# Kernel optimization log

Measured on AMD Instinct MI355X. Metric: run time of the kernel, lower is better.

The kernel has to match this reference:

```python
import jax, jax.numpy as jnp
import numpy as np

D_MODEL = 768
N_HEADS = 12
HEAD_DIM = D_MODEL // N_HEADS
FFN_DIM = 3072
MAX_WAVELENGTH = 10000.0
ROPE_PERCENT = 0.5
NORM_EPS = 1e-5


def setup_inputs() -> dict:
    key = jax.random.key(0)
    ks = jax.random.split(key, 12)
    B, C, S = 2, 16, 128
    init = lambda k, shape: (jax.random.normal(k, shape, dtype=jnp.float32) * 0.02)
    return {
        "hidden_state": jax.random.normal(ks[0], (B, C, S, D_MODEL), dtype=jnp.float32),
        "wq": init(ks[1], (D_MODEL, D_MODEL)), "bq": jnp.zeros((D_MODEL,), jnp.float32),
        "wk": init(ks[2], (D_MODEL, D_MODEL)), "bk": jnp.zeros((D_MODEL,), jnp.float32),
        "wv": init(ks[3], (D_MODEL, D_MODEL)), "bv": jnp.zeros((D_MODEL,), jnp.float32),
        "wo": init(ks[4], (D_MODEL, D_MODEL)), "bo": jnp.zeros((D_MODEL,), jnp.float32),
        "attn_biases": init(ks[5], (N_HEADS, 2)),
        "ln1_g": jnp.ones((D_MODEL,), jnp.float32), "ln1_b": jnp.zeros((D_MODEL,), jnp.float32),
        "ln3_g": jnp.ones((D_MODEL,), jnp.float32), "ln3_b": jnp.zeros((D_MODEL,), jnp.float32),
        "w1": init(ks[6], (D_MODEL, FFN_DIM)), "b1": jnp.zeros((FFN_DIM,), jnp.float32),
        "w2": init(ks[7], (FFN_DIM, D_MODEL)), "b2": jnp.zeros((D_MODEL,), jnp.float32),
    }


def _layernorm(x, g, b):
    mu = jnp.mean(x, axis=-1, keepdims=True)
    var = jnp.mean(jnp.square(x - mu), axis=-1, keepdims=True)
    return (x - mu) * jax.lax.rsqrt(var + NORM_EPS) * g + b


def _apply_p_rope(x, positions):
    # x: [B, H, T, head_dim]; p-RoPE: only rope_percent of frequency bands rotate.
    half = HEAD_DIM // 2
    rope_angles = int(ROPE_PERCENT * HEAD_DIM) // 2  # 16
    fraction = 2.0 * jnp.arange(rope_angles, dtype=jnp.float32) / HEAD_DIM
    timescale = jnp.concatenate([
        MAX_WAVELENGTH ** fraction,
        jnp.full((half - rope_angles,), jnp.inf, dtype=jnp.float32),
    ])  # [half]
    angles = positions[:, None].astype(jnp.float32) / timescale[None, :]  # [T, half]
    sin = jnp.sin(angles)[None, None]  # [1,1,T,half]
    cos = jnp.cos(angles)[None, None]
    x1, x2 = jnp.split(x, 2, axis=-1)
    return jnp.concatenate([x1 * cos - x2 * sin, x2 * cos + x1 * sin], axis=-1)


def _forward(hidden_state, wq, bq, wk, bk, wv, bv, wo, bo, attn_biases,
             ln1_g, ln1_b, ln3_g, ln3_b, w1, b1, w2, b2):
    B, C, S, D = hidden_state.shape
    T = C * S
    flat = hidden_state.reshape(B, T, D)

    # --- attention sublayer (pre-norm) ---
    ni = _layernorm(flat, ln1_g, ln1_b)
    scaling = HEAD_DIM ** -0.5
    q = (ni @ wq + bq) * scaling
    k = ni @ wk + bk
    v = ni @ wv + bv
    to_heads = lambda t: t.reshape(B, T, N_HEADS, HEAD_DIM).transpose(0, 2, 1, 3)
    q, k, v = to_heads(q), to_heads(k), to_heads(v)  # [B,H,T,hd]

    positions = jnp.arange(T)
    k = _apply_p_rope(k, positions)
    q = _apply_p_rope(q, positions)

    scores = jnp.einsum("bhtd,bhsd->bhts", q, k)  # [B,H,T,T]
    variate_ids = positions // S
    same = (variate_ids[:, None] == variate_ids[None, :]).astype(scores.dtype)  # [T,T]
    variate_bias = (same[None, :, :] * attn_biases[:, 0][:, None, None]
                    + (1.0 - same[None, :, :]) * attn_biases[:, 1][:, None, None])  # [H,T,T]
    scores = scores + variate_bias[None]
    probs = jax.nn.softmax(scores, axis=-1)
    attn = jnp.einsum("bhts,bhsd->bhtd", probs, v)
    attn = attn.transpose(0, 2, 1, 3).reshape(B, T, D)
    attn = attn @ wo + bo

    flat = flat + attn  # residual (pre-norm -> no post-norm here)

    # --- feed-forward sublayer (pre-norm) ---
    ff_in = _layernorm(flat, ln3_g, ln3_b)
    ff = jax.nn.gelu(ff_in @ w1 + b1, approximate=False) @ w2 + b2
    flat = flat + ff

    return flat.reshape(B, C, S, D)


def reference(hidden_state, wq, bq, wk, bk, wv, bv, wo, bo, attn_biases,
              ln1_g, ln1_b, ln3_g, ln3_b, w1, b1, w2, b2):
    return _forward(hidden_state, wq, bq, wk, bk, wv, bv, wo, bo, attn_biases,
                    ln1_g, ln1_b, ln3_g, ln3_b, w1, b1, w2, b2)
```

## Files before the change

kernel.cpp:

```cpp
#include <hip/hip_runtime.h>
#include <cmath>


typedef __bf16 bf16_t;
typedef bf16_t bf16x8 __attribute__((ext_vector_type(8)));
typedef float floatx4 __attribute__((ext_vector_type(4)));

#define MFMA(a, b, c) __builtin_amdgcn_mfma_f32_16x16x32_bf16((a), (b), (c), 0, 0, 0)
#define LOG2E 1.44269504088896340736f

__device__ __forceinline__ bf16_t f2bf(float f) { return (bf16_t)f; }

__device__ __forceinline__ void g2l16(const void* g, void* l) {
  __builtin_amdgcn_global_load_lds(
      (const __attribute__((address_space(1))) unsigned int*)g,
      (__attribute__((address_space(3))) unsigned int*)l, 16, 0, 0);
}

__device__ __forceinline__ void lds_fence() {
  asm volatile("s_waitcnt lgkmcnt(0)" ::: "memory");
}

struct PrepP {
  const float *wq, *wk, *wv, *wo, *w1, *w2;
  bf16_t *wqkvT, *woT, *w1T, *w2T;
  const float *hs, *g1, *be1;
  bf16_t* ni;
};

__global__ __launch_bounds__(256) void k_prep(PrepP p) {
  __shared__ float shm[32 * 33];
  const int bid = blockIdx.x;
  if (bid < 6912) {
    const float* in;
    bf16_t* out;
    int R, C, tx, ty;
    if (bid < 2304) {
      int m = bid / 576, lo = bid % 576;
      in = (m == 0) ? p.wq : (m == 1) ? p.wk : (m == 2) ? p.wv : p.wo;
      out = (m < 3) ? p.wqkvT + (size_t)m * 768 * 768 : p.woT;
      R = 768; C = 768; tx = lo % 24; ty = lo / 24;
    } else if (bid < 4608) {
      int lo = bid - 2304;
      in = p.w1; out = p.w1T; R = 768; C = 3072; tx = lo % 96; ty = lo / 96;
    } else {
      int lo = bid - 4608;
      in = p.w2; out = p.w2T; R = 3072; C = 768; tx = lo % 24; ty = lo / 24;
    }
    const int c0 = tx * 32, r0 = ty * 32;
    const int lx = threadIdx.x & 31, ly = threadIdx.x >> 5;
#pragma unroll
    for (int p4 = 0; p4 < 4; p4++) {
      int r = ly + p4 * 8;
      shm[r * 33 + lx] = in[(size_t)(r0 + r) * C + c0 + lx];
    }
    __syncthreads();
#pragma unroll
    for (int p4 = 0; p4 < 4; p4++) {
      int r = ly + p4 * 8;
      out[(size_t)(c0 + r) * R + r0 + lx] = f2bf(shm[lx * 33 + r]);
    }
  } else {
    const int row = bid - 6912;
    const float* xr = p.hs + (size_t)row * 768;
    const int t = threadIdx.x;
    float v0 = xr[t], v1 = xr[t + 256], v2 = xr[t + 512];
    float s = v0 + v1 + v2;
    float s2 = v0 * v0 + v1 * v1 + v2 * v2;
#pragma unroll
    for (int off = 32; off; off >>= 1) {
      s += __shfl_xor(s, off);
      s2 += __shfl_xor(s2, off);
    }
    const int w = t >> 6;
    if ((t & 63) == 0) { shm[w] = s; shm[4 + w] = s2; }
    __syncthreads();
    s = shm[0] + shm[1] + shm[2] + shm[3];
    s2 = shm[4] + shm[5] + shm[6] + shm[7];
    const float mu = s * (1.0f / 768.0f);
    const float var = s2 * (1.0f / 768.0f) - mu * mu;
    const float rstd = rsqrtf(var + 1e-5f);
    bf16_t* orow = p.ni + (size_t)row * 768;
    orow[t]       = f2bf((v0 - mu) * rstd * p.g1[t]       + p.be1[t]);
    orow[t + 256] = f2bf((v1 - mu) * rstd * p.g1[t + 256] + p.be1[t + 256]);
    orow[t + 512] = f2bf((v2 - mu) * rstd * p.g1[t + 512] + p.be1[t + 512]);
  }
}

__global__ __launch_bounds__(256) void k_layernorm(
    const float* __restrict__ x, const float* __restrict__ g,
    const float* __restrict__ b, bf16_t* __restrict__ out) {
  const int row = blockIdx.x;
  const float* xr = x + (size_t)row * 768;
  const int t = threadIdx.x;
  float v0 = xr[t], v1 = xr[t + 256], v2 = xr[t + 512];
  float s = v0 + v1 + v2;
  float s2 = v0 * v0 + v1 * v1 + v2 * v2;
#pragma unroll
  for (int off = 32; off; off >>= 1) {
    s += __shfl_xor(s, off);
    s2 += __shfl_xor(s2, off);
  }
  __shared__ float ra[4], rb[4];
  const int w = t >> 6;
  if ((t & 63) == 0) { ra[w] = s; rb[w] = s2; }
  __syncthreads();
  s = ra[0] + ra[1] + ra[2] + ra[3];
  s2 = rb[0] + rb[1] + rb[2] + rb[3];
  const float mu = s * (1.0f / 768.0f);
  const float var = s2 * (1.0f / 768.0f) - mu * mu;
  const float rstd = rsqrtf(var + 1e-5f);
  bf16_t* orow = out + (size_t)row * 768;
  orow[t]       = f2bf((v0 - mu) * rstd * g[t]       + b[t]);
  orow[t + 256] = f2bf((v1 - mu) * rstd * g[t + 256] + b[t + 256]);
  orow[t + 512] = f2bf((v2 - mu) * rstd * g[t + 512] + b[t + 512]);
}

struct GemmP {
  const bf16_t* A;
  const bf16_t* Bt;
  int M, N, K, mode;
  const float* bias0;
  const float* bias1;
  const float* bias2;
  float* outF;
  bf16_t* outB0;
  bf16_t* outB1;
  bf16_t* outB2;
};

__global__ __launch_bounds__(256, 3) void k_gemm(GemmP p) {
  __shared__ bf16_t lds[18432];
  const int tid = threadIdx.x;
  const int lane = tid & 63, wave = tid >> 6;
  const int quad = lane >> 4, l15 = lane & 15;
  const int wm = (wave >> 1) * 64, wn = (wave & 1) * 64;
  const int m0 = blockIdx.y * 128, n0 = blockIdx.x * 128;

  const char* gA[4];
  const char* gB[4];
#pragma unroll
  for (int pp = 0; pp < 4; pp++) {
    int slot = wave * 256 + pp * 64 + lane;
    int r = slot >> 3;
    int c8 = ((slot & 7) ^ (r & 7)) << 3;
    gA[pp] = (const char*)(p.A + (size_t)(m0 + r) * p.K + c8);
    gB[pp] = (const char*)(p.Bt + (size_t)(n0 + r) * p.K + c8);
  }

  int offA[4], offB[4];
#pragma unroll
  for (int i = 0; i < 4; i++) {
    int ra = wm + i * 16 + l15;
    offA[i] = ra * 64 + ((quad * 8) ^ ((ra & 7) << 3));
    int rb = wn + i * 16 + l15;
    offB[i] = rb * 64 + ((quad * 8) ^ ((rb & 7) << 3));
  }

  const floatx4 z4 = {0.f, 0.f, 0.f, 0.f};
  floatx4 acc[4][4];
#pragma unroll
  for (int i = 0; i < 4; i++)
#pragma unroll
    for (int j = 0; j < 4; j++) acc[i][j] = z4;

  const int KT = p.K >> 6;
  bf16_t* Ad = lds + wave * 2048;
  bf16_t* Bd = lds + 8192 + wave * 2048;

  for (int kt = 0; kt < KT; kt++) {
    const size_t kb = (size_t)kt * 128;
#pragma unroll
    for (int pp = 0; pp < 4; pp++) {
      g2l16(gA[pp] + kb, Ad + pp * 512);
      g2l16(gB[pp] + kb, Bd + pp * 512);
    }
    __syncthreads();
#pragma unroll
    for (int ks = 0; ks < 2; ks++) {
      bf16x8 af[4], bfr[4];
#pragma unroll
      for (int i = 0; i < 4; i++) {
        af[i] = *(const bf16x8*)(lds + (offA[i] ^ (ks * 32)));
        bfr[i] = *(const bf16x8*)(lds + 8192 + (offB[i] ^ (ks * 32)));
      }
#pragma unroll
      for (int i = 0; i < 4; i++)
#pragma unroll
        for (int j = 0; j < 4; j++) acc[i][j] = MFMA(af[i], bfr[j], acc[i][j]);
    }
    __syncthreads();
  }

  char* scr = (char*)lds + wave * 9216;

  if (p.mode == 0) {
    const int gnw = n0 + wn;
    const int region = gnw / 768;
    const int rem = gnw - region * 768;
    const int h = rem >> 6;
    const int b = (m0 + wm) >> 11;
    const int t0 = (m0 + wm) & 2047;
    const float* bias = (region == 0) ? p.bias0 : (region == 1 ? p.bias1 : p.bias2);
    float bb[4];
#pragma unroll
    for (int j = 0; j < 4; j++) bb[j] = bias[h * 64 + j * 16 + l15];
    bf16_t* sb = (bf16_t*)scr;
    if (region < 2) {
      const float scale = (region == 0) ? 0.125f * LOG2E : 1.0f;
      const float inv_ts = exp2f(-(float)l15 * (13.287712379549449f / 32.0f));
#pragma unroll
      for (int i = 0; i < 4; i++) {
#pragma unroll
        for (int reg = 0; reg < 4; reg++) {
          int tl = i * 16 + quad * 4 + reg;
          float sn, cs;
          __sincosf((float)(t0 + tl) * inv_ts, &sn, &cs);
          float v0 = (acc[i][0][reg] + bb[0]) * scale;
          float v1 = (acc[i][1][reg] + bb[1]) * scale;
          float v2 = (acc[i][2][reg] + bb[2]) * scale;
          float v3 = (acc[i][3][reg] + bb[3]) * scale;
          sb[tl * 72 + l15]      = f2bf(v0 * cs - v2 * sn);
          sb[tl * 72 + 16 + l15] = f2bf(v1);
          sb[tl * 72 + 32 + l15] = f2bf(v2 * cs + v0 * sn);
          sb[tl * 72 + 48 + l15] = f2bf(v3);
        }
      }
      __syncthreads();
      bf16_t* outp = (region == 0) ? p.outB0 : p.outB1;
      bf16_t* ob = outp + (((size_t)(b * 12 + h) * 2048 + t0) << 6);
#pragma unroll
      for (int pp = 0; pp < 8; pp++) {
        int row = pp * 8 + (lane >> 3), ch = (lane & 7) << 3;
        *(bf16x8*)(ob + row * 64 + ch) = *(const bf16x8*)&sb[row * 72 + ch];
      }
    } else {
#pragma unroll
      for (int i = 0; i < 4; i++)
#pragma unroll
        for (int j = 0; j < 4; j++)
#pragma unroll
          for (int reg = 0; reg < 4; reg++)
            sb[(j * 16 + l15) * 72 + i * 16 + quad * 4 + reg] =
                f2bf(acc[i][j][reg] + bb[j]);
      __syncthreads();
      bf16_t* ob = p.outB2 + (((size_t)(b * 12 + h)) << 17) + t0;
#pragma unroll
      for (int pp = 0; pp < 8; pp++) {
        int d = pp * 8 + (lane >> 3), ch = (lane & 7) << 3;
        *(bf16x8*)(ob + (size_t)d * 2048 + ch) = *(const bf16x8*)&sb[d * 72 + ch];
      }
    }
  } else {
    bf16_t* sb = (bf16_t*)scr;
    float bb[4];
#pragma unroll
    for (int j = 0; j < 4; j++) bb[j] = p.bias0[n0 + wn + j * 16 + l15];
#pragma unroll
    for (int i = 0; i < 4; i++)
#pragma unroll
      for (int j = 0; j < 4; j++)
#pragma unroll
        for (int reg = 0; reg < 4; reg++) {
          int tl = i * 16 + quad * 4 + reg;
          float x = acc[i][j][reg] + bb[j];
          float gv = 0.5f * x * (1.0f + erff(x * 0.70710678118654752f));
          sb[tl * 72 + j * 16 + l15] = f2bf(gv);
        }
    __syncthreads();
#pragma unroll
    for (int pp = 0; pp < 8; pp++) {
      int row = pp * 8 + (lane >> 3), ch = (lane & 7) << 3;
      *(bf16x8*)(p.outB0 + (size_t)(m0 + wm + row) * p.N + n0 + wn + ch) =
          *(const bf16x8*)&sb[row * 72 + ch];
    }
  }
}

__global__ __launch_bounds__(256, 4) void k_gemm64(
    const bf16_t* __restrict__ A, const bf16_t* __restrict__ Bt, int N, int K,
    const float* __restrict__ bias, const float* __restrict__ resid,
    float* __restrict__ outF) {
  __shared__ bf16_t lds[16384];
  const int tid = threadIdx.x;
  const int lane = tid & 63, wave = tid >> 6;
  const int quad = lane >> 4, l15 = lane & 15;
  const int wm = (wave >> 1) * 32, wn = (wave & 1) * 32;
  const int m0 = blockIdx.y * 64, n0 = blockIdx.x * 64;

  const char* gA[4];
  const char* gB[4];
#pragma unroll
  for (int pp = 0; pp < 4; pp++) {
    int slot = wave * 256 + pp * 64 + lane;
    int r = slot >> 4;
    int c = ((slot & 15) ^ (r & 7)) << 3;
    gA[pp] = (const char*)(A + (size_t)(m0 + r) * K + c);
    gB[pp] = (const char*)(Bt + (size_t)(n0 + r) * K + c);
  }

  const floatx4 z4 = {0.f, 0.f, 0.f, 0.f};
  floatx4 acc[2][2];
#pragma unroll
  for (int i = 0; i < 2; i++)
#pragma unroll
    for (int j = 0; j < 2; j++) acc[i][j] = z4;

  const int KT = K >> 7;
  bf16_t* Ad = lds + wave * 2048;
  bf16_t* Bd = lds + 8192 + wave * 2048;

  for (int kt = 0; kt < KT; kt++) {
    const size_t kb = (size_t)kt * 256;
#pragma unroll
    for (int pp = 0; pp < 4; pp++) {
      g2l16(gA[pp] + kb, Ad + pp * 512);
      g2l16(gB[pp] + kb, Bd + pp * 512);
    }
    __syncthreads();
#pragma unroll
    for (int ks = 0; ks < 4; ks++) {
      bf16x8 af[2], bfr[2];
#pragma unroll
      for (int i = 0; i < 2; i++) {
        int ra = wm + i * 16 + l15;
        af[i] = *(const bf16x8*)(lds + ra * 128 +
                                 (((ks * 4 + quad) ^ (ra & 7)) << 3));
        int rb = wn + i * 16 + l15;
        bfr[i] = *(const bf16x8*)(lds + 8192 + rb * 128 +
                                  (((ks * 4 + quad) ^ (rb & 7)) << 3));
      }
#pragma unroll
      for (int i = 0; i < 2; i++)
#pragma unroll
        for (int j = 0; j < 2; j++) acc[i][j] = MFMA(af[i], bfr[j], acc[i][j]);
    }
    __syncthreads();
  }

  float* s4 = (float*)lds + wave * 1024;
#pragma unroll
  for (int i = 0; i < 2; i++)
#pragma unroll
    for (int j = 0; j < 2; j++)
#pragma unroll
      for (int reg = 0; reg < 4; reg++)
        s4[(i * 16 + quad * 4 + reg) * 32 + j * 16 + l15] = acc[i][j][reg];
  __syncthreads();
#pragma unroll
  for (int pp = 0; pp < 4; pp++) {
    int row = pp * 8 + (lane >> 3);
    int c4 = (lane & 7) * 4;
    floatx4 v = *(const floatx4*)&s4[row * 32 + c4];
    size_t goff = (size_t)(m0 + wm + row) * N + n0 + wn + c4;
    floatx4 rv = *(const floatx4*)(resid + goff);
    floatx4 bv = *(const floatx4*)(bias + n0 + wn + c4);
    *(floatx4*)(outF + goff) = v + rv + bv;
  }
}

__global__ __launch_bounds__(256, 3) void k_flash(
    const bf16_t* __restrict__ qh, const bf16_t* __restrict__ kh,
    const bf16_t* __restrict__ vt, const float* __restrict__ ab,
    bf16_t* __restrict__ attnA) {
  __shared__ bf16_t sm[20480];
  bf16_t* lK = sm;
  bf16_t* lV = sm + 8192;
  bf16_t* lP = sm + 16384;

  const int tid = threadIdx.x, lane = tid & 63, wave = tid >> 6;
  const int quad = lane >> 4, l15 = lane & 15;
  const int qtile = blockIdx.x, bh = blockIdx.y;
  const int h = bh % 12, bq = bh / 12;
  const int qr0 = qtile * 64 + wave * 16;

  const bf16_t* Qb = qh + (size_t)bh * 2048 * 64;
  const bf16_t* Kb = kh + (size_t)bh * 2048 * 64;
  const bf16_t* Vb = vt + (size_t)bh * 64 * 2048;

  const char* gK[2];
  const char* gV[2];
#pragma unroll
  for (int pp = 0; pp < 2; pp++) {
    int slot = wave * 128 + pp * 64 + lane;
    int r = slot >> 3;
    int c8 = ((slot & 7) ^ (r & 7)) << 3;
    gK[pp] = (const char*)(Kb + r * 64 + c8);
    gV[pp] = (const char*)(Vb + (size_t)r * 2048 + c8);
  }

  bf16x8 qf[2];
#pragma unroll
  for (int ks = 0; ks < 2; ks++)
    qf[ks] = *(const bf16x8*)(Qb + (size_t)(qr0 + l15) * 64 + ks * 32 + quad * 8);

  int offK[4];
#pragma unroll
  for (int t4 = 0; t4 < 4; t4++) {
    int sr = t4 * 16 + l15;
    offK[t4] = sr * 64 + ((quad * 8) ^ ((sr & 7) << 3));
  }
  const int offP = l15 * 64 + ((quad * 8) ^ ((l15 & 7) << 3));

  const floatx4 z4 = {0.f, 0.f, 0.f, 0.f};
  float l_all[4] = {0.f, 0.f, 0.f, 0.f};
  floatx4 oacc[4];
#pragma unroll
  for (int dt = 0; dt < 4; dt++) oacc[dt] = z4;

  const float bc_same = ab[h * 2] * LOG2E;
  const float bc_diff = ab[h * 2 + 1] * LOG2E;
  const int myv = qtile >> 1;

  {
    bf16_t* K0 = lK + wave * 1024;
    bf16_t* V0 = lV + wave * 1024;
#pragma unroll
    for (int pp = 0; pp < 2; pp++) {
      g2l16(gK[pp], K0 + pp * 512);
      g2l16(gV[pp], V0 + pp * 512);
    }
  }
  __syncthreads();

  for (int kv = 0; kv < 32; kv++) {
    const int cur = kv & 1;
    if (kv + 1 < 32) {
      bf16_t* K1 = lK + (cur ^ 1) * 4096 + wave * 1024;
      bf16_t* V1 = lV + (cur ^ 1) * 4096 + wave * 1024;
      const size_t kb = (size_t)(kv + 1) * 8192, vb = (size_t)(kv + 1) * 128;
#pragma unroll
      for (int pp = 0; pp < 2; pp++) {
        g2l16(gK[pp] + kb, K1 + pp * 512);
        g2l16(gV[pp] + vb, V1 + pp * 512);
      }
    }
    const bf16_t* K0 = lK + cur * 4096;
    const bf16_t* V0 = lV + cur * 4096;

    floatx4 sacc[4] = {z4, z4, z4, z4};
#pragma unroll
    for (int ks = 0; ks < 2; ks++)
#pragma unroll
      for (int ct = 0; ct < 4; ct++)
        sacc[ct] = MFMA(qf[ks], *(const bf16x8*)(K0 + (offK[ct] ^ (ks * 32))),
                        sacc[ct]);

    const float bc = ((kv >> 1) == myv) ? bc_same : bc_diff;
#pragma unroll
    for (int ct = 0; ct < 4; ct++)
#pragma unroll
      for (int reg = 0; reg < 4; reg++) {
        float pv = exp2f(sacc[ct][reg] + bc);
        sacc[ct][reg] = pv;
        l_all[reg] += pv;
      }

    bf16_t* myP = lP + wave * 1024;
#pragma unroll
    for (int ct = 0; ct < 4; ct++)
#pragma unroll
      for (int reg = 0; reg < 4; reg++) {
        int r = quad * 4 + reg, s = ct * 16 + l15;
        myP[r * 64 + (((s >> 3) ^ (r & 7)) << 3) + (s & 7)] =
            f2bf(sacc[ct][reg]);
      }
    lds_fence();

#pragma unroll
    for (int ks = 0; ks < 2; ks++) {
      bf16x8 pf = *(const bf16x8*)(myP + (offP ^ (ks * 32)));
#pragma unroll
      for (int dt = 0; dt < 4; dt++)
        oacc[dt] = MFMA(pf, *(const bf16x8*)(V0 + (offK[dt] ^ (ks * 32))),
                        oacc[dt]);
    }
    __syncthreads();
  }

  float inv_l[4];
#pragma unroll
  for (int reg = 0; reg < 4; reg++) {
    float la = l_all[reg];
    la += __shfl_xor(la, 1); la += __shfl_xor(la, 2);
    la += __shfl_xor(la, 4); la += __shfl_xor(la, 8);
    inv_l[reg] = 1.0f / la;
  }

  bf16_t* myP = lP + wave * 1024;
#pragma unroll
  for (int dt = 0; dt < 4; dt++)
#pragma unroll
    for (int reg = 0; reg < 4; reg++)
      myP[(quad * 4 + reg) * 64 + dt * 16 + l15] =
          f2bf(oacc[dt][reg] * inv_l[reg]);
  __syncthreads();
#pragma unroll
  for (int pp = 0; pp < 2; pp++) {
    int row = pp * 8 + (lane >> 3), ch = (lane & 7) << 3;
    *(bf16x8*)(attnA + ((size_t)(bq * 2048 + qr0 + row)) * 768 + h * 64 + ch) =
        *(const bf16x8*)&myP[row * 64 + ch];
  }
}

extern "C" void kernel_launch(void* const* d_in, const int* in_sizes, int n_in,
                              void* d_out, int out_size, void* d_ws,
                              size_t ws_size, hipStream_t stream) {
  const float* hs  = (const float*)d_in[0];
  const float* wq  = (const float*)d_in[1];
  const float* bq  = (const float*)d_in[2];
  const float* wk  = (const float*)d_in[3];
  const float* bk  = (const float*)d_in[4];
  const float* wv  = (const float*)d_in[5];
  const float* bv  = (const float*)d_in[6];
  const float* wo  = (const float*)d_in[7];
  const float* bo  = (const float*)d_in[8];
  const float* ab  = (const float*)d_in[9];
  const float* g1  = (const float*)d_in[10];
  const float* be1 = (const float*)d_in[11];
  const float* g3  = (const float*)d_in[12];
  const float* be3 = (const float*)d_in[13];
  const float* w1  = (const float*)d_in[14];
  const float* b1  = (const float*)d_in[15];
  const float* w2  = (const float*)d_in[16];
  const float* b2  = (const float*)d_in[17];

  char* ws = (char*)d_ws;
  size_t off = 0;
  auto alloc = [&](size_t bytes) -> void* {
    void* p = ws + off;
    off += (bytes + 255) & ~(size_t)255;
    return p;
  };
  bf16_t* wqkvT = (bf16_t*)alloc((size_t)2304 * 768 * 2);
  bf16_t* woT   = (bf16_t*)alloc((size_t)768 * 768 * 2);
  bf16_t* w1T   = (bf16_t*)alloc((size_t)3072 * 768 * 2);
  bf16_t* w2T   = (bf16_t*)alloc((size_t)768 * 3072 * 2);
  bf16_t* ni    = (bf16_t*)alloc((size_t)4096 * 768 * 2);
  bf16_t* qhB   = (bf16_t*)alloc((size_t)24 * 2048 * 64 * 2);
  bf16_t* khB   = (bf16_t*)alloc((size_t)24 * 2048 * 64 * 2);
  bf16_t* vtB   = (bf16_t*)alloc((size_t)24 * 64 * 2048 * 2);
  bf16_t* attnA = (bf16_t*)alloc((size_t)4096 * 768 * 2);
  float*  resid1 = (float*)alloc((size_t)4096 * 768 * 4);
  bf16_t* ffn1o = qhB;

  PrepP pp = {wq, wk, wv, wo, w1, w2, wqkvT, woT, w1T, w2T, hs, g1, be1, ni};
  k_prep<<<11008, 256, 0, stream>>>(pp);

  GemmP gqkv = {ni, wqkvT, 4096, 2304, 768, 0,
                bq, bk, bv, nullptr, qhB, khB, vtB};
  k_gemm<<<dim3(18, 32), 256, 0, stream>>>(gqkv);

  k_flash<<<dim3(32, 24), 256, 0, stream>>>(qhB, khB, vtB, ab, attnA);

  k_gemm64<<<dim3(12, 64), 256, 0, stream>>>(attnA, woT, 768, 768, bo, hs,
                                             resid1);

  k_layernorm<<<4096, 256, 0, stream>>>(resid1, g3, be3, ni);

  GemmP gf1 = {ni, w1T, 4096, 3072, 768, 2,
               b1, nullptr, nullptr, nullptr, ffn1o, nullptr, nullptr};
  k_gemm<<<dim3(24, 32), 256, 0, stream>>>(gf1);

  k_gemm64<<<dim3(12, 64), 256, 0, stream>>>(ffn1o, w2T, 768, 3072, b2,
                                             resid1, (float*)d_out);
}
```

Baseline: 290.8 us.

## Rewrite flash attention with 32x32 MFMA, two-wave blocks, transposed S

The flash kernel now uses 32x32x16 bf16 MFMA instructions with 128-thread blocks, where each wave owns 32 query rows. Scores are computed transposed (K as the A operand), so each lane holds one query column and the row-sum reduction shrinks to a single shuffle. The K/V double buffering is removed in favour of a single buffer with a barrier per tile, and P is packed and stored as bf16x4. Fewer, larger MFMAs and a smaller LDS footprint are traded against losing the overlap of global loads with compute.

```diff
diff --git a/kernel.cpp b/kernel.cpp
--- a/kernel.cpp
+++ b/kernel.cpp
@@ -3,10 +3,13 @@
 
 
 typedef __bf16 bf16_t;
+typedef bf16_t bf16x4 __attribute__((ext_vector_type(4)));
 typedef bf16_t bf16x8 __attribute__((ext_vector_type(8)));
 typedef float floatx4 __attribute__((ext_vector_type(4)));
+typedef float floatx16 __attribute__((ext_vector_type(16)));
 
 #define MFMA(a, b, c) __builtin_amdgcn_mfma_f32_16x16x32_bf16((a), (b), (c), 0, 0, 0)
+#define MFMA32(a, b, c) __builtin_amdgcn_mfma_f32_32x32x16_bf16((a), (b), (c), 0, 0, 0)
 #define LOG2E 1.44269504088896340736f
 
 __device__ __forceinline__ bf16_t f2bf(float f) { return (bf16_t)f; }
@@ -359,147 +362,119 @@
   }
 }
 
-__global__ __launch_bounds__(256, 3) void k_flash(
+__global__ __launch_bounds__(128, 2) void k_flash(
     const bf16_t* __restrict__ qh, const bf16_t* __restrict__ kh,
     const bf16_t* __restrict__ vt, const float* __restrict__ ab,
     bf16_t* __restrict__ attnA) {
-  __shared__ bf16_t sm[20480];
+  __shared__ bf16_t sm[12288];
   bf16_t* lK = sm;
-  bf16_t* lV = sm + 8192;
-  bf16_t* lP = sm + 16384;
+  bf16_t* lV = sm + 4096;
+  bf16_t* lP = sm + 8192;
 
   const int tid = threadIdx.x, lane = tid & 63, wave = tid >> 6;
-  const int quad = lane >> 4, l15 = lane & 15;
+  const int l31 = lane & 31, lh = lane >> 5;
+  const int sw = l31 & 7;
   const int qtile = blockIdx.x, bh = blockIdx.y;
   const int h = bh % 12, bq = bh / 12;
-  const int qr0 = qtile * 64 + wave * 16;
+  const int qw = qtile * 64 + wave * 32;
 
   const bf16_t* Qb = qh + (size_t)bh * 2048 * 64;
   const bf16_t* Kb = kh + (size_t)bh * 2048 * 64;
   const bf16_t* Vb = vt + (size_t)bh * 64 * 2048;
 
-  const char* gK[2];
-  const char* gV[2];
-#pragma unroll
-  for (int pp = 0; pp < 2; pp++) {
-    int slot = wave * 128 + pp * 64 + lane;
+  const char* gK[4];
+  const char* gV[4];
+#pragma unroll
+  for (int pp = 0; pp < 4; pp++) {
+    int slot = pp * 128 + tid;
     int r = slot >> 3;
     int c8 = ((slot & 7) ^ (r & 7)) << 3;
     gK[pp] = (const char*)(Kb + r * 64 + c8);
     gV[pp] = (const char*)(Vb + (size_t)r * 2048 + c8);
   }
 
-  bf16x8 qf[2];
-#pragma unroll
-  for (int ks = 0; ks < 2; ks++)
-    qf[ks] = *(const bf16x8*)(Qb + (size_t)(qr0 + l15) * 64 + ks * 32 + quad * 8);
-
-  int offK[4];
-#pragma unroll
-  for (int t4 = 0; t4 < 4; t4++) {
-    int sr = t4 * 16 + l15;
-    offK[t4] = sr * 64 + ((quad * 8) ^ ((sr & 7) << 3));
-  }
-  const int offP = l15 * 64 + ((quad * 8) ^ ((l15 & 7) << 3));
-
-  const floatx4 z4 = {0.f, 0.f, 0.f, 0.f};
-  float l_all[4] = {0.f, 0.f, 0.f, 0.f};
-  floatx4 oacc[4];
-#pragma unroll
-  for (int dt = 0; dt < 4; dt++) oacc[dt] = z4;
+  bf16x8 qf[4];
+#pragma unroll
+  for (int ks = 0; ks < 4; ks++)
+    qf[ks] = *(const bf16x8*)(Qb + (size_t)(qw + l31) * 64 + ks * 16 + lh * 8);
+
+  const floatx16 z16 = {0.f, 0.f, 0.f, 0.f, 0.f, 0.f, 0.f, 0.f,
+                        0.f, 0.f, 0.f, 0.f, 0.f, 0.f, 0.f, 0.f};
+  floatx16 oacc0 = z16, oacc1 = z16;
+  float l_part = 0.f;
 
   const float bc_same = ab[h * 2] * LOG2E;
   const float bc_diff = ab[h * 2 + 1] * LOG2E;
   const int myv = qtile >> 1;
 
-  {
-    bf16_t* K0 = lK + wave * 1024;
-    bf16_t* V0 = lV + wave * 1024;
-#pragma unroll
-    for (int pp = 0; pp < 2; pp++) {
-      g2l16(gK[pp], K0 + pp * 512);
-      g2l16(gV[pp], V0 + pp * 512);
-    }
-  }
-  __syncthreads();
+  bf16_t* myP = lP + wave * 2048;
 
   for (int kv = 0; kv < 32; kv++) {
-    const int cur = kv & 1;
-    if (kv + 1 < 32) {
-      bf16_t* K1 = lK + (cur ^ 1) * 4096 + wave * 1024;
-      bf16_t* V1 = lV + (cur ^ 1) * 4096 + wave * 1024;
-      const size_t kb = (size_t)(kv + 1) * 8192, vb = (size_t)(kv + 1) * 128;
-#pragma unroll
-      for (int pp = 0; pp < 2; pp++) {
-        g2l16(gK[pp] + kb, K1 + pp * 512);
-        g2l16(gV[pp] + vb, V1 + pp * 512);
+    const size_t kb = (size_t)kv * 8192, vb = (size_t)kv * 128;
+#pragma unroll
+    for (int pp = 0; pp < 4; pp++) {
+      g2l16(gK[pp] + kb, lK + pp * 1024 + wave * 512);
+      g2l16(gV[pp] + vb, lV + pp * 1024 + wave * 512);
+    }
+    __syncthreads();
+
+    floatx16 sacc0 = z16, sacc1 = z16;
+#pragma unroll
+    for (int ks = 0; ks < 4; ks++) {
+      const int ch = ((2 * ks + lh) ^ sw) << 3;
+      sacc0 = MFMA32(*(const bf16x8*)(lK + l31 * 64 + ch), qf[ks], sacc0);
+      sacc1 = MFMA32(*(const bf16x8*)(lK + (32 + l31) * 64 + ch), qf[ks], sacc1);
+    }
+
+    const float bc = ((kv >> 1) == myv) ? bc_same : bc_diff;
+#pragma unroll
+    for (int st = 0; st < 2; st++) {
+      const floatx16& sv = st ? sacc1 : sacc0;
+#pragma unroll
+      for (int g = 0; g < 4; g++) {
+        bf16x4 pk;
+#pragma unroll
+        for (int r = 0; r < 4; r++) {
+          float pv = exp2f(sv[g * 4 + r] + bc);
+          l_part += pv;
+          pk[r] = f2bf(pv);
+        }
+        *(bf16x4*)(myP + l31 * 64 + (((st * 4 + g) ^ sw) << 3) + 4 * lh) = pk;
       }
     }
-    const bf16_t* K0 = lK + cur * 4096;
-    const bf16_t* V0 = lV + cur * 4096;
-
-    floatx4 sacc[4] = {z4, z4, z4, z4};
-#pragma unroll
-    for (int ks = 0; ks < 2; ks++)
-#pragma unroll
-      for (int ct = 0; ct < 4; ct++)
-        sacc[ct] = MFMA(qf[ks], *(const bf16x8*)(K0 + (offK[ct] ^ (ks * 32))),
-                        sacc[ct]);
-
-    const float bc = ((kv >> 1) == myv) ? bc_same : bc_diff;
-#pragma unroll
-    for (int ct = 0; ct < 4; ct++)
-#pragma unroll
-      for (int reg = 0; reg < 4; reg++) {
-        float pv = exp2f(sacc[ct][reg] + bc);
-        sacc[ct][reg] = pv;
-        l_all[reg] += pv;
-      }
-
-    bf16_t* myP = lP + wave * 1024;
-#pragma unroll
-    for (int ct = 0; ct < 4; ct++)
-#pragma unroll
-      for (int reg = 0; reg < 4; reg++) {
-        int r = quad * 4 + reg, s = ct * 16 + l15;
-        myP[r * 64 + (((s >> 3) ^ (r & 7)) << 3) + (s & 7)] =
-            f2bf(sacc[ct][reg]);
-      }
     lds_fence();
 
 #pragma unroll
-    for (int ks = 0; ks < 2; ks++) {
-      bf16x8 pf = *(const bf16x8*)(myP + (offP ^ (ks * 32)));
-#pragma unroll
-      for (int dt = 0; dt < 4; dt++)
-        oacc[dt] = MFMA(pf, *(const bf16x8*)(V0 + (offK[dt] ^ (ks * 32))),
-                        oacc[dt]);
-    }
-    __syncthreads();
-  }
-
-  float inv_l[4];
-#pragma unroll
-  for (int reg = 0; reg < 4; reg++) {
-    float la = l_all[reg];
-    la += __shfl_xor(la, 1); la += __shfl_xor(la, 2);
-    la += __shfl_xor(la, 4); la += __shfl_xor(la, 8);
-    inv_l[reg] = 1.0f / la;
-  }
-
-  bf16_t* myP = lP + wave * 1024;
-#pragma unroll
-  for (int dt = 0; dt < 4; dt++)
-#pragma unroll
-    for (int reg = 0; reg < 4; reg++)
-      myP[(quad * 4 + reg) * 64 + dt * 16 + l15] =
-          f2bf(oacc[dt][reg] * inv_l[reg]);
-  __syncthreads();
-#pragma unroll
-  for (int pp = 0; pp < 2; pp++) {
-    int row = pp * 8 + (lane >> 3), ch = (lane & 7) << 3;
-    *(bf16x8*)(attnA + ((size_t)(bq * 2048 + qr0 + row)) * 768 + h * 64 + ch) =
-        *(const bf16x8*)&myP[row * 64 + ch];
+    for (int ks = 0; ks < 4; ks++) {
+      const int ch = ((2 * ks + lh) ^ sw) << 3;
+      const bf16x8 pf = *(const bf16x8*)(myP + l31 * 64 + ch);
+      oacc0 = MFMA32(*(const bf16x8*)(lV + l31 * 64 + ch), pf, oacc0);
+      oacc1 = MFMA32(*(const bf16x8*)(lV + (32 + l31) * 64 + ch), pf, oacc1);
+    }
+    __syncthreads();
+  }
+
+  const float l_tot = l_part + __shfl_xor(l_part, 32);
+  const float inv = 1.0f / l_tot;
+
+  lds_fence();
+#pragma unroll
+  for (int dt = 0; dt < 2; dt++) {
+    const floatx16& ov = dt ? oacc1 : oacc0;
+#pragma unroll
+    for (int g = 0; g < 4; g++) {
+      bf16x4 pk;
+#pragma unroll
+      for (int r = 0; r < 4; r++) pk[r] = f2bf(ov[g * 4 + r] * inv);
+      *(bf16x4*)(myP + l31 * 64 + (((dt * 4 + g) ^ sw) << 3) + 4 * lh) = pk;
+    }
+  }
+  lds_fence();
+#pragma unroll
+  for (int ps = 0; ps < 4; ps++) {
+    int rr = ps * 8 + (lane >> 3), c = lane & 7;
+    bf16x8 v = *(const bf16x8*)(myP + rr * 64 + (((c ^ (rr & 7)) << 3)));
+    *(bf16x8*)(attnA + ((size_t)(bq * 2048 + qw + rr)) * 768 + h * 64 + c * 8) = v;
   }
 }
 
@@ -551,7 +526,7 @@
                 bq, bk, bv, nullptr, qhB, khB, vtB};
   k_gemm<<<dim3(18, 32), 256, 0, stream>>>(gqkv);
 
-  k_flash<<<dim3(32, 24), 256, 0, stream>>>(qhB, khB, vtB, ab, attnA);
+  k_flash<<<dim3(32, 24), 128, 0, stream>>>(qhB, khB, vtB, ab, attnA);
 
   k_gemm64<<<dim3(12, 64), 256, 0, stream>>>(attnA, woT, 768, 768, bo, hs,
                                              resid1);
```

Result: slower. 302.9 us (+4.2%).

## Split-K the FFN down-projection with atomic accumulation and remap block order

Applied to the files above, without the earlier changes.

Replaces the 64x64-tile down-projection GEMM (K=3072) with a 128x128-tile split-K kernel that divides K into four chunks and accumulates partial results into the output with float atomics. The first chunk also adds bias and residual, and the output is zeroed by a memset. Separately, block indices in the GEMM kernels are remapped column-major so consecutive blocks share B tiles, aiming for better L2 reuse. The split-K path adds atomic traffic, an extra memset, and a single-buffered K loop with no load/compute overlap.

```diff
diff --git a/kernel.cpp b/kernel.cpp
--- a/kernel.cpp
+++ b/kernel.cpp
@@ -135,7 +135,9 @@
   const int lane = tid & 63, wave = tid >> 6;
   const int quad = lane >> 4, l15 = lane & 15;
   const int wm = (wave >> 1) * 64, wn = (wave & 1) * 64;
-  const int m0 = blockIdx.y * 128, n0 = blockIdx.x * 128;
+  const int id = blockIdx.y * gridDim.x + blockIdx.x;
+  const int bx = id / gridDim.y, by = id % gridDim.y;
+  const int m0 = by * 128, n0 = bx * 128;
 
   const char* gA[4];
   const char* gB[4];
@@ -286,7 +288,9 @@
   const int lane = tid & 63, wave = tid >> 6;
   const int quad = lane >> 4, l15 = lane & 15;
   const int wm = (wave >> 1) * 32, wn = (wave & 1) * 32;
-  const int m0 = blockIdx.y * 64, n0 = blockIdx.x * 64;
+  const int id = blockIdx.y * gridDim.x + blockIdx.x;
+  const int bx = id / gridDim.y, by = id % gridDim.y;
+  const int m0 = by * 64, n0 = bx * 64;
 
   const char* gA[4];
   const char* gB[4];
@@ -357,6 +361,91 @@
     floatx4 bv = *(const floatx4*)(bias + n0 + wn + c4);
     *(floatx4*)(outF + goff) = v + rv + bv;
   }
+}
+
+__global__ __launch_bounds__(256, 3) void k_gemm_sk(
+    const bf16_t* __restrict__ A, const bf16_t* __restrict__ Bt, int N, int K,
+    int chunk, const float* __restrict__ bias, const float* __restrict__ resid,
+    float* __restrict__ outF) {
+  __shared__ bf16_t lds[16384];
+  const int tid = threadIdx.x;
+  const int lane = tid & 63, wave = tid >> 6;
+  const int quad = lane >> 4, l15 = lane & 15;
+  const int wm = (wave >> 1) * 64, wn = (wave & 1) * 64;
+  const int id = blockIdx.y * gridDim.x + blockIdx.x;
+  const int bx = id / gridDim.y, by = id % gridDim.y;
+  const int m0 = by * 128, n0 = bx * 128;
+  const int k0 = blockIdx.z * chunk;
+
+  const char* gA[4];
+  const char* gB[4];
+#pragma unroll
+  for (int pp = 0; pp < 4; pp++) {
+    int slot = wave * 256 + pp * 64 + lane;
+    int r = slot >> 3;
+    int c8 = ((slot & 7) ^ (r & 7)) << 3;
+    gA[pp] = (const char*)(A + (size_t)(m0 + r) * K + k0 + c8);
+    gB[pp] = (const char*)(Bt + (size_t)(n0 + r) * K + k0 + c8);
+  }
+
+  int offA[4], offB[4];
+#pragma unroll
+  for (int i = 0; i < 4; i++) {
+    int ra = wm + i * 16 + l15;
+    offA[i] = ra * 64 + ((quad * 8) ^ ((ra & 7) << 3));
+    int rb = wn + i * 16 + l15;
+    offB[i] = rb * 64 + ((quad * 8) ^ ((rb & 7) << 3));
+  }
+
+  const floatx4 z4 = {0.f, 0.f, 0.f, 0.f};
+  floatx4 acc[4][4];
+#pragma unroll
+  for (int i = 0; i < 4; i++)
+#pragma unroll
+    for (int j = 0; j < 4; j++) acc[i][j] = z4;
+
+  const int KT = chunk >> 6;
+  bf16_t* Ad = lds + wave * 2048;
+  bf16_t* Bd = lds + 8192 + wave * 2048;
+
+  for (int kt = 0; kt < KT; kt++) {
+    const size_t kb = (size_t)kt * 128;
+#pragma unroll
+    for (int pp = 0; pp < 4; pp++) {
+      g2l16(gA[pp] + kb, Ad + pp * 512);
+      g2l16(gB[pp] + kb, Bd + pp * 512);
+    }
+    __syncthreads();
+#pragma unroll
+    for (int ks = 0; ks < 2; ks++) {
+      bf16x8 af[4], bfr[4];
+#pragma unroll
+      for (int i = 0; i < 4; i++) {
+        af[i] = *(const bf16x8*)(lds + (offA[i] ^ (ks * 32)));
+        bfr[i] = *(const bf16x8*)(lds + 8192 + (offB[i] ^ (ks * 32)));
+      }
+#pragma unroll
+      for (int i = 0; i < 4; i++)
+#pragma unroll
+        for (int j = 0; j < 4; j++) acc[i][j] = MFMA(af[i], bfr[j], acc[i][j]);
+    }
+    __syncthreads();
+  }
+
+  const bool first = (blockIdx.z == 0);
+#pragma unroll
+  for (int i = 0; i < 4; i++)
+#pragma unroll
+    for (int j = 0; j < 4; j++)
+#pragma unroll
+      for (int reg = 0; reg < 4; reg++) {
+        int row = m0 + wm + i * 16 + quad * 4 + reg;
+        int col = n0 + wn + j * 16 + l15;
+        size_t goff = (size_t)row * N + col;
+        float v = acc[i][j][reg];
+        if (first) v += bias[col] + resid[goff];
+        unsafeAtomicAdd(outF + goff, v);
+      }
 }
 
 __global__ __launch_bounds__(256, 3) void k_flash(
@@ -544,6 +633,8 @@
   float*  resid1 = (float*)alloc((size_t)4096 * 768 * 4);
   bf16_t* ffn1o = qhB;
 
+  hipMemsetAsync(d_out, 0, (size_t)4096 * 768 * 4, stream);
+
   PrepP pp = {wq, wk, wv, wo, w1, w2, wqkvT, woT, w1T, w2T, hs, g1, be1, ni};
   k_prep<<<11008, 256, 0, stream>>>(pp);
 
@@ -562,6 +653,6 @@
                b1, nullptr, nullptr, nullptr, ffn1o, nullptr, nullptr};
   k_gemm<<<dim3(24, 32), 256, 0, stream>>>(gf1);
 
-  k_gemm64<<<dim3(12, 64), 256, 0, stream>>>(ffn1o, w2T, 768, 3072, b2,
-                                             resid1, (float*)d_out);
-}
+  k_gemm_sk<<<dim3(6, 32, 4), 256, 0, stream>>>(ffn1o, w2T, 768, 3072, 768,
+                                                b2, resid1, (float*)d_out);
+}
```

Measured after the change: 311.6 us. 7.2% more time.

## Split flash attention KV range across waves with per-wave private buffers

Applied to the files above, without the earlier changes.

The attention kernel now has each of the four waves handle all 64 query rows of the tile. Each wave processes a disjoint 16-key slice of every KV block, using its own LDS region for K, V and P. The block-wide barriers per KV step are gone: each wave prefetches its own slice, waits with vmcnt, and only does the PV MFMA every second step. Partial outputs and row sums are combined across waves through LDS at the end. This raises LDS use and register pressure (occupancy hint drops from 3 to 2) and adds a bf16 partial-sum reduction, which could cost precision.

```diff
diff --git a/kernel.cpp b/kernel.cpp
--- a/kernel.cpp
+++ b/kernel.cpp
@@ -19,6 +19,9 @@
 
 __device__ __forceinline__ void lds_fence() {
   asm volatile("s_waitcnt lgkmcnt(0)" ::: "memory");
+}
+__device__ __forceinline__ void wait_vm4() {
+  asm volatile("s_waitcnt vmcnt(4)" ::: "memory");
 }
 
 struct PrepP {
@@ -359,148 +362,187 @@
   }
 }
 
-__global__ __launch_bounds__(256, 3) void k_flash(
+__global__ __launch_bounds__(256, 2) void k_flash(
     const bf16_t* __restrict__ qh, const bf16_t* __restrict__ kh,
     const bf16_t* __restrict__ vt, const float* __restrict__ ab,
     bf16_t* __restrict__ attnA) {
-  __shared__ bf16_t sm[20480];
-  bf16_t* lK = sm;
-  bf16_t* lV = sm + 8192;
-  bf16_t* lP = sm + 16384;
+  __shared__ bf16_t sm[35328];
 
   const int tid = threadIdx.x, lane = tid & 63, wave = tid >> 6;
   const int quad = lane >> 4, l15 = lane & 15;
   const int qtile = blockIdx.x, bh = blockIdx.y;
   const int h = bh % 12, bq = bh / 12;
-  const int qr0 = qtile * 64 + wave * 16;
-
-  const bf16_t* Qb = qh + (size_t)bh * 2048 * 64;
-  const bf16_t* Kb = kh + (size_t)bh * 2048 * 64;
-  const bf16_t* Vb = vt + (size_t)bh * 64 * 2048;
+  const int myv = qtile >> 1;
+
+  bf16_t* wb = sm + wave * 8704;
+  bf16_t* Kb0 = wb;
+  bf16_t* Vs = wb + 2048;
+  bf16_t* Pb = wb + 6144;
+
+  const bf16_t* Qg = qh + ((size_t)bh * 2048 + qtile * 64) * 64;
+  const bf16_t* Kg = kh + ((size_t)bh * 2048 + wave * 16) * 64;
 
   const char* gK[2];
+#pragma unroll
+  for (int i = 0; i < 2; i++) {
+    int sl = i * 8 + (lane >> 3);
+    int cs = (lane & 7) ^ (sl & 7);
+    gK[i] = (const char*)(Kg + sl * 64 + cs * 8);
+  }
   const char* gV[2];
 #pragma unroll
-  for (int pp = 0; pp < 2; pp++) {
-    int slot = wave * 128 + pp * 64 + lane;
-    int r = slot >> 3;
-    int c8 = ((slot & 7) ^ (r & 7)) << 3;
-    gK[pp] = (const char*)(Kb + r * 64 + c8);
-    gV[pp] = (const char*)(Vb + (size_t)r * 2048 + c8);
-  }
-
-  bf16x8 qf[2];
+  for (int i = 0; i < 2; i++) {
+    int d = i * 32 + (lane >> 1);
+    int hs = (lane & 1) ^ ((d >> 2) & 1);
+    gV[i] = (const char*)(vt + ((size_t)(bh * 64 + d)) * 2048 + wave * 16 + hs * 8);
+  }
+
+  bf16x8 qf[4][2];
+#pragma unroll
+  for (int mt = 0; mt < 4; mt++)
+#pragma unroll
+    for (int ks = 0; ks < 2; ks++)
+      qf[mt][ks] = *(const bf16x8*)(Qg + (size_t)(mt * 16 + l15) * 64 +
+                                    ks * 32 + quad * 8);
+
+  int offKr[2];
 #pragma unroll
   for (int ks = 0; ks < 2; ks++)
-    qf[ks] = *(const bf16x8*)(Qb + (size_t)(qr0 + l15) * 64 + ks * 32 + quad * 8);
-
-  int offK[4];
-#pragma unroll
-  for (int t4 = 0; t4 < 4; t4++) {
-    int sr = t4 * 16 + l15;
-    offK[t4] = sr * 64 + ((quad * 8) ^ ((sr & 7) << 3));
-  }
-  const int offP = l15 * 64 + ((quad * 8) ^ ((l15 & 7) << 3));
+    offKr[ks] = l15 * 64 + ((((ks << 2) + quad) ^ (l15 & 7)) << 3);
+  int offV[4];
+#pragma unroll
+  for (int nt = 0; nt < 4; nt++) {
+    int d = nt * 16 + l15;
+    offV[nt] = (quad >> 1) * 1024 + d * 16 +
+               (((quad & 1) ^ ((d >> 2) & 1)) << 3);
+  }
 
   const floatx4 z4 = {0.f, 0.f, 0.f, 0.f};
-  float l_all[4] = {0.f, 0.f, 0.f, 0.f};
-  floatx4 oacc[4];
-#pragma unroll
-  for (int dt = 0; dt < 4; dt++) oacc[dt] = z4;
+  floatx4 oacc[4][4];
+  float l_lane[4][4];
+#pragma unroll
+  for (int mt = 0; mt < 4; mt++)
+#pragma unroll
+    for (int nt = 0; nt < 4; nt++) oacc[mt][nt] = z4;
+#pragma unroll
+  for (int mt = 0; mt < 4; mt++)
+#pragma unroll
+    for (int r = 0; r < 4; r++) l_lane[mt][r] = 0.f;
 
   const float bc_same = ab[h * 2] * LOG2E;
   const float bc_diff = ab[h * 2 + 1] * LOG2E;
-  const int myv = qtile >> 1;
-
-  {
-    bf16_t* K0 = lK + wave * 1024;
-    bf16_t* V0 = lV + wave * 1024;
-#pragma unroll
-    for (int pp = 0; pp < 2; pp++) {
-      g2l16(gK[pp], K0 + pp * 512);
-      g2l16(gV[pp], V0 + pp * 512);
-    }
-  }
+
+  g2l16(gK[0], Kb0);
+  g2l16(gK[1], Kb0 + 512);
+  g2l16(gV[0], Vs);
+  g2l16(gV[1], Vs + 512);
+
+  for (int kv = 0; kv < 32; kv++) {
+    const int nkv = (kv + 1) & 31;
+    {
+      const size_t kbK = (size_t)nkv * 8192, kbV = (size_t)nkv * 128;
+      bf16_t* Kd = Kb0 + (nkv & 1) * 1024;
+      bf16_t* Vd = Vs + ((((nkv >> 1) & 1) << 1) + (nkv & 1)) * 1024;
+      g2l16(gK[0] + kbK, Kd);
+      g2l16(gK[1] + kbK, Kd + 512);
+      g2l16(gV[0] + kbV, Vd);
+      g2l16(gV[1] + kbV, Vd + 512);
+    }
+    wait_vm4();
+
+    const bf16_t* Kc = Kb0 + (kv & 1) * 1024;
+    floatx4 sacc[4] = {z4, z4, z4, z4};
+#pragma unroll
+    for (int ks = 0; ks < 2; ks++) {
+      const bf16x8 kf = *(const bf16x8*)(Kc + offKr[ks]);
+#pragma unroll
+      for (int mt = 0; mt < 4; mt++)
+        sacc[mt] = MFMA(qf[mt][ks], kf, sacc[mt]);
+    }
+
+    const float bc = ((kv >> 1) == myv) ? bc_same : bc_diff;
+    const int pw = (kv & 1) * 16 + l15;
+#pragma unroll
+    for (int mt = 0; mt < 4; mt++)
+#pragma unroll
+      for (int reg = 0; reg < 4; reg++) {
+        float pv = exp2f(sacc[mt][reg] + bc);
+        l_lane[mt][reg] += pv;
+        Pb[(mt * 16 + quad * 4 + reg) * 40 + pw] = f2bf(pv);
+      }
+
+    if (kv & 1) {
+      lds_fence();
+      bf16x8 pf[4];
+#pragma unroll
+      for (int mt = 0; mt < 4; mt++)
+        pf[mt] = *(const bf16x8*)(Pb + (mt * 16 + l15) * 40 + quad * 8);
+      const int vb = ((kv >> 1) & 1) * 2048;
+#pragma unroll
+      for (int nt = 0; nt < 4; nt++) {
+        const bf16x8 vf = *(const bf16x8*)(Vs + vb + offV[nt]);
+#pragma unroll
+        for (int mt = 0; mt < 4; mt++)
+          oacc[mt][nt] = MFMA(pf[mt], vf, oacc[mt][nt]);
+      }
+    }
+  }
+
+#pragma unroll
+  for (int mt = 0; mt < 4; mt++)
+#pragma unroll
+    for (int reg = 0; reg < 4; reg++) {
+      float v = l_lane[mt][reg];
+      v += __shfl_xor(v, 1);
+      v += __shfl_xor(v, 2);
+      v += __shfl_xor(v, 4);
+      v += __shfl_xor(v, 8);
+      l_lane[mt][reg] = v;
+    }
+  float* lred = (float*)(sm + 34816);
+  if (l15 == 0) {
+#pragma unroll
+    for (int mt = 0; mt < 4; mt++)
+#pragma unroll
+      for (int reg = 0; reg < 4; reg++)
+        lred[wave * 64 + mt * 16 + quad * 4 + reg] = l_lane[mt][reg];
+  }
+#pragma unroll
+  for (int mt = 0; mt < 4; mt++)
+#pragma unroll
+    for (int nt = 0; nt < 4; nt++)
+#pragma unroll
+      for (int reg = 0; reg < 4; reg++)
+        wb[(mt * 16 + quad * 4 + reg) * 64 + nt * 16 + l15] =
+            f2bf(oacc[mt][nt][reg]);
   __syncthreads();
 
-  for (int kv = 0; kv < 32; kv++) {
-    const int cur = kv & 1;
-    if (kv + 1 < 32) {
-      bf16_t* K1 = lK + (cur ^ 1) * 4096 + wave * 1024;
-      bf16_t* V1 = lV + (cur ^ 1) * 4096 + wave * 1024;
-      const size_t kb = (size_t)(kv + 1) * 8192, vb = (size_t)(kv + 1) * 128;
-#pragma unroll
-      for (int pp = 0; pp < 2; pp++) {
-        g2l16(gK[pp] + kb, K1 + pp * 512);
-        g2l16(gV[pp] + vb, V1 + pp * 512);
-      }
-    }
-    const bf16_t* K0 = lK + cur * 4096;
-    const bf16_t* V0 = lV + cur * 4096;
-
-    floatx4 sacc[4] = {z4, z4, z4, z4};
-#pragma unroll
-    for (int ks = 0; ks < 2; ks++)
-#pragma unroll
-      for (int ct = 0; ct < 4; ct++)
-        sacc[ct] = MFMA(qf[ks], *(const bf16x8*)(K0 + (offK[ct] ^ (ks * 32))),
-                        sacc[ct]);
-
-    const float bc = ((kv >> 1) == myv) ? bc_same : bc_diff;
-#pragma unroll
-    for (int ct = 0; ct < 4; ct++)
-#pragma unroll
-      for (int reg = 0; reg < 4; reg++) {
-        float pv = exp2f(sacc[ct][reg] + bc);
-        sacc[ct][reg] = pv;
-        l_all[reg] += pv;
-      }
-
-    bf16_t* myP = lP + wave * 1024;
-#pragma unroll
-    for (int ct = 0; ct < 4; ct++)
-#pragma unroll
-      for (int reg = 0; reg < 4; reg++) {
-        int r = quad * 4 + reg, s = ct * 16 + l15;
-        myP[r * 64 + (((s >> 3) ^ (r & 7)) << 3) + (s & 7)] =
-            f2bf(sacc[ct][reg]);
-      }
-    lds_fence();
-
-#pragma unroll
-    for (int ks = 0; ks < 2; ks++) {
-      bf16x8 pf = *(const bf16x8*)(myP + (offP ^ (ks * 32)));
-#pragma unroll
-      for (int dt = 0; dt < 4; dt++)
-        oacc[dt] = MFMA(pf, *(const bf16x8*)(V0 + (offK[dt] ^ (ks * 32))),
-                        oacc[dt]);
-    }
-    __syncthreads();
-  }
-
-  float inv_l[4];
-#pragma unroll
-  for (int reg = 0; reg < 4; reg++) {
-    float la = l_all[reg];
-    la += __shfl_xor(la, 1); la += __shfl_xor(la, 2);
-    la += __shfl_xor(la, 4); la += __shfl_xor(la, 8);
-    inv_l[reg] = 1.0f / la;
-  }
-
-  bf16_t* myP = lP + wave * 1024;
-#pragma unroll
-  for (int dt = 0; dt < 4; dt++)
-#pragma unroll
-    for (int reg = 0; reg < 4; reg++)
-      myP[(quad * 4 + reg) * 64 + dt * 16 + l15] =
-          f2bf(oacc[dt][reg] * inv_l[reg]);
-  __syncthreads();
-#pragma unroll
-  for (int pp = 0; pp < 2; pp++) {
-    int row = pp * 8 + (lane >> 3), ch = (lane & 7) << 3;
-    *(bf16x8*)(attnA + ((size_t)(bq * 2048 + qr0 + row)) * 768 + h * 64 + ch) =
-        *(const bf16x8*)&myP[row * 64 + ch];
-  }
+  const int q = tid >> 2, dg = (tid & 3) * 16;
+  const float inv =
+      1.0f / (lred[q] + lred[64 + q] + lred[128 + q] + lred[192 + q]);
+  float o[16];
+#pragma unroll
+  for (int j = 0; j < 16; j++) o[j] = 0.f;
+#pragma unroll
+  for (int w = 0; w < 4; w++) {
+    const bf16x8 a = *(const bf16x8*)(sm + w * 8704 + q * 64 + dg);
+    const bf16x8 b = *(const bf16x8*)(sm + w * 8704 + q * 64 + dg + 8);
+#pragma unroll
+    for (int j = 0; j < 8; j++) {
+      o[j] += (float)a[j];
+      o[8 + j] += (float)b[j];
+    }
+  }
+  bf16x8 r0, r1;
+#pragma unroll
+  for (int j = 0; j < 8; j++) {
+    r0[j] = f2bf(o[j] * inv);
+    r1[j] = f2bf(o[8 + j] * inv);
+  }
+  bf16_t* outp =
+      attnA + ((size_t)(bq * 2048 + qtile * 64 + q)) * 768 + h * 64 + dg;
+  *(bf16x8*)outp = r0;
+  *(bf16x8*)(outp + 8) = r1;
 }
 
 extern "C" void kernel_launch(void* const* d_in, const int* in_sizes, int n_in,
```

Result: no change. 287.7 us (-1.1%).
